# Kernel tuning notes

Hardware: AMD Instinct MI355X
Metric: run time of the kernel (lower is better)

The kernel has to match this reference:

```python
import jax, jax.numpy as jnp
import numpy as np

# --- fixed model configuration (from init_kwargs) ---
NX, NY, NU, NP = 8, 8, 2, 5
DELTA = 0.01
PHO, CP, AR, AB = 5.0, 6.0, 3.0, 3.0
KR, KB, TD, QR, QB = 2.5, 1.5, 300.0, 200.0, 200.0
CAF, TF = 6.0, 320.0
YMEAN = jnp.array([50.0, 1.0, 0.5, 313.0, 50.0, 1.0, 0.5, 313.0], jnp.float32)
YSTD = jnp.array([2.0, 0.2, 0.1, 4.0, 2.0, 0.2, 0.1, 4.0], jnp.float32)
UMEAN = jnp.array([10.0, 5.0], jnp.float32)
USTD = jnp.array([1.0, 0.5], jnp.float32)


def _fg(x, u):
    """Grey-box CSTR+flash ODE RHS. x: [B,8] scaled, u: [B,2] scaled."""
    x = x * YSTD + YMEAN
    u = u * USTD + UMEAN
    Hr, CAr, CBr, Tr = x[..., 0:1], x[..., 1:2], x[..., 2:3], x[..., 3:4]
    Hb, CAb, CBb, Tb = x[..., 4:5], x[..., 5:6], x[..., 6:7], x[..., 7:8]
    F, D = u[..., 0:1], u[..., 1:2]
    Fr = KR * jnp.sqrt(Hr)
    Fb = KB * jnp.sqrt(Hb)
    dHr = (F + D - Fr) / AR
    dCAr = (F * (CAF - CAr) - D * CAr) / (AR * Hr)
    dCBr = (-F * CBr - D * CBr) / (AR * Hr)
    dTr = (F * (TF - Tr) + D * (TD - Tr)) / (AR * Hr) + QR / (PHO * AR * CP * Hr)
    dHb = (Fr - Fb - D) / AB
    dCAb = (Fr * (CAr - CAb) + D * CAb) / (AB * Hb)
    dCBb = (Fr * (CBr - CBb) + D * CBb) / (AB * Hb)
    dTb = Fr * (Tr - Tb) / (AB * Hb) + QB / (PHO * AB * CP * Hb)
    xdot = jnp.concatenate([dHr, dCAr, dCBr, dTr, dHb, dCAb, dCBb, dTb], axis=-1)
    return xdot / YSTD


def setup_inputs() -> dict:
    key = jax.random.key(0)
    ks = jax.random.split(key, 6)
    B, T = 2048, 128
    d_in, d_h = NX + NP * (NY + NU) + NU, 128  # 60, 128
    useq = jax.random.normal(ks[0], (B, T, NU), jnp.float32)
    xGz0 = jax.random.normal(ks[1], (B, NX + NP * (NY + NU)), jnp.float32)
    W1 = jax.random.normal(ks[2], (d_in, d_h), jnp.float32) * (1.0 / np.sqrt(d_in))
    b1 = jnp.zeros((d_h,), jnp.float32)
    W2 = jax.random.normal(ks[3], (d_h, d_h), jnp.float32) * (1.0 / np.sqrt(d_h))
    b2 = jnp.zeros((d_h,), jnp.float32)
    W3 = jax.random.normal(ks[4], (d_h, NX), jnp.float32) * (1.0 / np.sqrt(d_h))
    b3 = jnp.zeros((NX,), jnp.float32)
    return {"useq": useq, "xGz0": xGz0, "W1": W1, "b1": b1,
            "W2": W2, "b2": b2, "W3": W3, "b3": b3}


def reference(useq, xGz0, W1, b1, W2, b2, W3, b3):
    def fnn(inp):
        h = jnp.tanh(inp @ W1 + b1)
        h = jnp.tanh(h @ W2 + b2)
        return h @ W3 + b3

    def interp(yfull):  # [B,(Np+1)*Ny] -> [B,Np*Ny]
        B = yfull.shape[0]
        y = yfull.reshape(B, NP + 1, NY)
        return (0.5 * (y[:, :-1] + y[:, 1:])).reshape(B, NP * NY)

    def step(xGz, u):
        xG = xGz[:, :NX]
        z = xGz[:, NX:]
        ypseq = z[:, :NP * NY]
        upseq = z[:, NP * NY:]
        # k1
        k1 = _fg(xG, u) + fnn(jnp.concatenate((xG, z, u), axis=-1))
        # interpolated half-step past sequence
        yp_interp = interp(jnp.concatenate((ypseq, xG), axis=-1))
        z_half = jnp.concatenate((yp_interp, upseq), axis=-1)
        x2 = xG + DELTA * (k1 / 2)
        k2 = _fg(x2, u) + fnn(jnp.concatenate((x2, z_half, u), axis=-1))
        x3 = xG + DELTA * (k2 / 2)
        k3 = _fg(x3, u) + fnn(jnp.concatenate((x3, z_half, u), axis=-1))
        yp_shift = jnp.concatenate((ypseq[:, NY:], xG), axis=-1)
        z_full = jnp.concatenate((yp_shift, upseq), axis=-1)
        x4 = xG + DELTA * k3
        k4 = _fg(x4, u) + fnn(jnp.concatenate((x4, z_full, u), axis=-1))
        y = xG
        xGplus = xG + (DELTA / 6) * (k1 + 2 * k2 + 2 * k3 + k4)
        zplus = jnp.concatenate((yp_shift, upseq[:, NU:], u), axis=-1)
        return jnp.concatenate((xGplus, zplus), axis=-1), y

    u_t = jnp.swapaxes(useq, 0, 1)  # [T,B,Nu]
    _, ys = jax.lax.scan(step, xGz0, u_t)  # ys: [T,B,Ny]
    return jnp.swapaxes(ys, 0, 1)  # [B,T,Ny]
```

## Files before the change

kernel.cpp:

```cpp
#include <hip/hip_runtime.h>
#include <math.h>

#define BLOCK 512
#define ROWS 8

typedef __attribute__((ext_vector_type(8))) short s16x8;
typedef __attribute__((ext_vector_type(4))) float f32x4;

static constexpr int O_H1   = 0;
static constexpr int O_H2   = 1088;
static constexpr int O_SU   = 2176;
static constexpr int O_PRIV = 4224;
static constexpr int PRIV_DW = 640;
static constexpr int LDSN  = O_PRIV + 8 * PRIV_DW;

__device__ __forceinline__ unsigned short f2bf(float f) {
  unsigned u = __float_as_uint(f);
  return (unsigned short)((u + 0x7fffu + ((u >> 16) & 1u)) >> 16);
}
__device__ __forceinline__ unsigned cvt_pk_bf16(float lo, float hi) {
  unsigned r;
  asm("v_cvt_pk_bf16_f32 %0, %1, %2" : "=v"(r) : "v"(lo), "v"(hi));
  return r;
}
__device__ __forceinline__ float tanh_fast(float x) {
  float e = __builtin_amdgcn_exp2f(x * 2.88539008177792681f);
  return fmaf(-2.f, __builtin_amdgcn_rcpf(e + 1.f), 1.f);
}

#define MFMA16(A, B, C) __builtin_amdgcn_mfma_f32_16x16x32_bf16((A), (B), (C), 0, 0, 0)

#define PACK_OUT(C, BV, DST) {                        \
  float t0_ = tanh_fast((C)[0] + (BV).x);             \
  float t1_ = tanh_fast((C)[1] + (BV).y);             \
  float t2_ = tanh_fast((C)[2] + (BV).z);             \
  float t3_ = tanh_fast((C)[3] + (BV).w);             \
  uint2 pk_; pk_.x = cvt_pk_bf16(t0_, t1_);           \
  pk_.y = cvt_pk_bf16(t2_, t3_);                      \
  *(uint2*)(DST) = pk_; }

extern "C" __global__ void __launch_bounds__(BLOCK, 1)
cstr_rk4_mfma6(const float* __restrict__ useq, const float* __restrict__ xGz0,
               const float* __restrict__ W1, const float* __restrict__ b1,
               const float* __restrict__ W2, const float* __restrict__ b2,
               const float* __restrict__ W3, const float* __restrict__ b3,
               float* __restrict__ out)
{
  extern __shared__ float smf[];
  unsigned short* h1h = (unsigned short*)(smf + O_H1);
  unsigned*       h1u = (unsigned*)(smf + O_H1);
  unsigned short* h2h = (unsigned short*)(smf + O_H2);
  unsigned*       h2u = (unsigned*)(smf + O_H2);
  float* su = smf + O_SU;

  const int tid  = threadIdx.x;
  const int w    = tid >> 6;
  const int l    = tid & 63;
  const int nn   = l & 15;
  const int hh   = l >> 4;
  const int r    = l >> 3;
  const int c    = l & 7;
  const int base = blockIdx.x * ROWS;

  float* wp_ = smf + O_PRIV + w * PRIV_DW;
  unsigned short* inhp = (unsigned short*)wp_;
  float* xmp = wp_ + 576;

  for (int i = tid; i < ROWS * 256; i += BLOCK) su[i] = useq[(size_t)base * 256 + i];
  for (int i = l; i < 16 * 72; i += 64) {
    int n_ = i / 72, k = i % 72;
    unsigned short v = 0;
    if (n_ < ROWS) {
      if (k < 58)      v = f2bf(xGz0[(size_t)(base + n_) * 58 + k]);
      else if (k < 60) v = f2bf(useq[(size_t)(base + n_) * 256 + (k - 58)]);
    }
    inhp[i] = v;
  }
  xmp[l] = xGz0[(size_t)(base + r) * 58 + c];

  const size_t rowb = (size_t)(base + r) * 58;
  float xg  = xGz0[rowb + c];
  float yp0 = xGz0[rowb + 8 + c],  yp1 = xGz0[rowb + 16 + c];
  float yp2 = xGz0[rowb + 24 + c], yp3 = xGz0[rowb + 32 + c];
  float yp4 = xGz0[rowb + 40 + c];
  float upA = xGz0[rowb + 48 + c];
  float upB = (c < 2) ? xGz0[rowb + 56 + c] : 0.f;
  float b3r = b3[c];
  float kacc = 0.f;

  const int j = 16 * w + nn;
  s16x8 a10, a11, a20, a21, a22, a23, a30, a31, a32, a33;
  #pragma unroll
  for (int i = 0; i < 8; ++i) {
    int k0 = 8 * hh + i, k1 = 32 + 8 * hh + i;
    a10[i] = (short)f2bf(W1[k0 * 128 + j]);
    a11[i] = (short)((k1 < 60) ? f2bf(W1[k1 * 128 + j]) : 0);
    a20[i] = (short)f2bf(W2[(     8 * hh + i) * 128 + j]);
    a21[i] = (short)f2bf(W2[(32 + 8 * hh + i) * 128 + j]);
    a22[i] = (short)f2bf(W2[(64 + 8 * hh + i) * 128 + j]);
    a23[i] = (short)f2bf(W2[(96 + 8 * hh + i) * 128 + j]);
    unsigned short z0 = 0, z1 = 0, z2 = 0, z3 = 0;
    if (nn < 8) {
      z0 = f2bf(W3[(     8 * hh + i) * 8 + nn]);
      z1 = f2bf(W3[(32 + 8 * hh + i) * 8 + nn]);
      z2 = f2bf(W3[(64 + 8 * hh + i) * 8 + nn]);
      z3 = f2bf(W3[(96 + 8 * hh + i) * 8 + nn]);
    }
    a30[i] = (short)z0; a31[i] = (short)z1; a32[i] = (short)z2; a33[i] = (short)z3;
  }
  const float4 bva = *(const float4*)(b1 + 16 * w + 4 * hh);
  const float4 bvb = *(const float4*)(b2 + 16 * w + 4 * hh);

  __syncthreads();

  const int srcl = ((c >> 2) << 4) + r;

  #pragma unroll 1
  for (int t = 0; t < 128; ++t) {
    const float u0r = su[r * 256 + 2 * t];
    const float u1r = su[r * 256 + 2 * t + 1];
    if (w == 0) out[((size_t)(base + r) * 128 + t) * 8 + c] = xg;

    #pragma unroll
    for (int s = 0; s < 4; ++s) {
      {
        s16x8 bb0 = *(const s16x8*)(inhp + nn * 72 + 8 * hh);
        s16x8 bb1 = *(const s16x8*)(inhp + nn * 72 + 32 + 8 * hh);
        f32x4 c1 = (f32x4){0.f, 0.f, 0.f, 0.f};
        c1 = MFMA16(a10, bb0, c1);
        c1 = MFMA16(a11, bb1, c1);
        PACK_OUT(c1, bva, h1u + nn * 68 + 8 * w + 2 * hh);
      }
      __syncthreads();

      {
        const unsigned short* h1row = h1h + nn * 136;
        s16x8 q0 = *(const s16x8*)(h1row +  0 + 8 * hh);
        s16x8 q1 = *(const s16x8*)(h1row + 32 + 8 * hh);
        s16x8 q2 = *(const s16x8*)(h1row + 64 + 8 * hh);
        s16x8 q3 = *(const s16x8*)(h1row + 96 + 8 * hh);
        f32x4 c2 = (f32x4){0.f, 0.f, 0.f, 0.f};
        c2 = MFMA16(a20, q0, c2); c2 = MFMA16(a21, q1, c2);
        c2 = MFMA16(a22, q2, c2); c2 = MFMA16(a23, q3, c2);
        PACK_OUT(c2, bvb, h2u + nn * 68 + 8 * w + 2 * hh);
      }
      __syncthreads();

      f32x4 c3 = (f32x4){0.f, 0.f, 0.f, 0.f};
      {
        const unsigned short* h2row = h2h + nn * 136;
        s16x8 p0 = *(const s16x8*)(h2row +  0 + 8 * hh);
        s16x8 p1 = *(const s16x8*)(h2row + 32 + 8 * hh);
        s16x8 p2 = *(const s16x8*)(h2row + 64 + 8 * hh);
        s16x8 p3 = *(const s16x8*)(h2row + 96 + 8 * hh);
        c3 = MFMA16(a30, p0, c3); c3 = MFMA16(a31, p1, c3);
        c3 = MFMA16(a32, p2, c3); c3 = MFMA16(a33, p3, c3);
      }
      float v0 = __shfl(c3[0], srcl);
      float v1 = __shfl(c3[1], srcl);
      float v2 = __shfl(c3[2], srcl);
      float v3 = __shfl(c3[3], srcl);
      {
        float nv = b3r + ((c & 2) ? ((c & 1) ? v3 : v2)
                                  : ((c & 1) ? v1 : v0));
        float4 xa = *(const float4*)(xmp + r * 8);
        float4 xb = *(const float4*)(xmp + r * 8 + 4);
        float Hr  = fmaf(xa.x, 2.f, 50.f),  CAr = fmaf(xa.y, 0.2f, 1.f);
        float CBr = fmaf(xa.z, 0.1f, 0.5f), Tr  = fmaf(xa.w, 4.f, 313.f);
        float Hb  = fmaf(xb.x, 2.f, 50.f),  CAb = fmaf(xb.y, 0.2f, 1.f);
        float CBb = fmaf(xb.z, 0.1f, 0.5f), Tb  = fmaf(xb.w, 4.f, 313.f);
        float F = u0r + 10.f, D = fmaf(u1r, 0.5f, 5.f);
        float Fr = 2.5f * sqrtf(Hr), Fb = 1.5f * sqrtf(Hb);
        float rH = __builtin_amdgcn_rcpf(3.f * Hr);
        float rB = __builtin_amdgcn_rcpf(3.f * Hb);
        float k0 = (F + D - Fr) * (1.f / 6.f);
        float k1 = (F * (6.f - CAr) - D * CAr) * (5.f * rH);
        float k2 = (-(F + D) * CBr) * (10.f * rH);
        float k3 = (F * (320.f - Tr) + D * (300.f - Tr)) * (0.25f * rH) + (5.f / 3.f) * rH;
        float k4 = (Fr - Fb - D) * (1.f / 6.f);
        float k5 = (Fr * (CAr - CAb) + D * CAb) * (5.f * rB);
        float k6 = (Fr * (CBr - CBb) + D * CBb) * (10.f * rB);
        float k7 = Fr * (Tr - Tb) * (0.25f * rB) + (5.f / 3.f) * rB;
        float fgc = (c & 4) ? ((c & 2) ? ((c & 1) ? k7 : k6) : ((c & 1) ? k5 : k4))
                            : ((c & 2) ? ((c & 1) ? k3 : k2) : ((c & 1) ? k1 : k0));
        float kv = fgc + nv;
        float cc;
        if (s == 0)      { kacc = kv;                  cc = fmaf(kv, 0.005f, xg); }
        else if (s == 1) { kacc = fmaf(kv, 2.f, kacc); cc = fmaf(kv, 0.005f, xg); }
        else if (s == 2) { kacc = fmaf(kv, 2.f, kacc); cc = fmaf(kv, 0.01f,  xg); }
        else             { xg = fmaf(kacc + kv, 0.01f / 6.f, xg); cc = xg; }
        xmp[r * 8 + c] = cc;
        inhp[r * 72 + c] = f2bf(cc);

        if (s == 0) {
          inhp[r * 72 +  8 + c] = f2bf(0.5f * (yp0 + yp1));
          inhp[r * 72 + 16 + c] = f2bf(0.5f * (yp1 + yp2));
          inhp[r * 72 + 24 + c] = f2bf(0.5f * (yp2 + yp3));
          inhp[r * 72 + 32 + c] = f2bf(0.5f * (yp3 + yp4));
          inhp[r * 72 + 40 + c] = f2bf(0.5f * (yp4 + xg));
        } else if (s == 2) {
          inhp[r * 72 +  8 + c] = f2bf(yp1);
          inhp[r * 72 + 16 + c] = f2bf(yp2);
          inhp[r * 72 + 24 + c] = f2bf(yp3);
          inhp[r * 72 + 32 + c] = f2bf(yp4);
          inhp[r * 72 + 40 + c] = f2bf(xg);
          yp0 = yp1; yp1 = yp2; yp2 = yp3; yp3 = yp4; yp4 = xg;
        } else if (s == 3) {
          float tA = __shfl(upA, r * 8 + ((c + 2) & 7));
          float tB = __shfl(upB, r * 8 + ((c >= 6) ? (c - 6) : 0));
          float nu = (c < 6) ? tA : tB;
          upA = nu;
          inhp[r * 72 + 48 + c] = f2bf(nu);
          if (c < 2) {
            float uv = (c == 0) ? u0r : u1r;
            upB = uv;
            inhp[r * 72 + 56 + c] = f2bf(uv);
            if (t < 127)
              inhp[r * 72 + 58 + c] = f2bf(su[r * 256 + 2 * (t + 1) + c]);
          }
        }
      }
    }
  }
}

extern "C" void kernel_launch(void* const* d_in, const int* in_sizes, int n_in,
                              void* d_out, int out_size, void* d_ws, size_t ws_size,
                              hipStream_t stream) {
  const float* useq = (const float*)d_in[0];
  const float* xGz0 = (const float*)d_in[1];
  const float* W1   = (const float*)d_in[2];
  const float* b1   = (const float*)d_in[3];
  const float* W2   = (const float*)d_in[4];
  const float* b2   = (const float*)d_in[5];
  const float* W3   = (const float*)d_in[6];
  const float* b3   = (const float*)d_in[7];
  float* out = (float*)d_out;

  size_t lds = (size_t)LDSN * sizeof(float);
  (void)hipFuncSetAttribute((const void*)cstr_rk4_mfma6,
                            hipFuncAttributeMaxDynamicSharedMemorySize, (int)lds);
  hipLaunchKernelGGL(cstr_rk4_mfma6, dim3(2048 / ROWS), dim3(BLOCK), lds, stream,
                     useq, xGz0, W1, b1, W2, b2, W3, b3, out);
}
```

Baseline: 541.6 us.

## Compute layer-3 and RK4 state update in one wave with shared input buffers

```diff
diff --git a/kernel.cpp b/kernel.cpp
--- a/kernel.cpp
+++ b/kernel.cpp
@@ -7,12 +7,12 @@
 typedef __attribute__((ext_vector_type(8))) short s16x8;
 typedef __attribute__((ext_vector_type(4))) float f32x4;
 
-static constexpr int O_H1   = 0;
-static constexpr int O_H2   = 1088;
-static constexpr int O_SU   = 2176;
-static constexpr int O_PRIV = 4224;
-static constexpr int PRIV_DW = 640;
-static constexpr int LDSN  = O_PRIV + 8 * PRIV_DW;
+static constexpr int O_H1  = 0;
+static constexpr int O_H2  = 1088;
+static constexpr int O_INH = 2176;
+static constexpr int O_XM  = 2752;
+static constexpr int O_SU  = 2816;
+static constexpr int LDSN  = 4896;
 
 __device__ __forceinline__ unsigned short f2bf(float f) {
   unsigned u = __float_as_uint(f);
@@ -40,7 +40,7 @@
   *(uint2*)(DST) = pk_; }
 
 extern "C" __global__ void __launch_bounds__(BLOCK, 1)
-cstr_rk4_mfma6(const float* __restrict__ useq, const float* __restrict__ xGz0,
+cstr_rk4_mfma7(const float* __restrict__ useq, const float* __restrict__ xGz0,
                const float* __restrict__ W1, const float* __restrict__ b1,
                const float* __restrict__ W2, const float* __restrict__ b2,
                const float* __restrict__ W3, const float* __restrict__ b3,
@@ -51,6 +51,8 @@
   unsigned*       h1u = (unsigned*)(smf + O_H1);
   unsigned short* h2h = (unsigned short*)(smf + O_H2);
   unsigned*       h2u = (unsigned*)(smf + O_H2);
+  unsigned short* inh = (unsigned short*)(smf + O_INH);
+  float* xm = smf + O_XM;
   float* su = smf + O_SU;
 
   const int tid  = threadIdx.x;
@@ -62,21 +64,20 @@
   const int c    = l & 7;
   const int base = blockIdx.x * ROWS;
 
-  float* wp_ = smf + O_PRIV + w * PRIV_DW;
-  unsigned short* inhp = (unsigned short*)wp_;
-  float* xmp = wp_ + 576;
-
-  for (int i = tid; i < ROWS * 256; i += BLOCK) su[i] = useq[(size_t)base * 256 + i];
-  for (int i = l; i < 16 * 72; i += 64) {
+  for (int i = tid; i < 8 * 260; i += BLOCK) {
+    int row = i / 260, col = i % 260;
+    su[i] = (col < 256) ? useq[(size_t)base * 256 + row * 256 + col] : 0.f;
+  }
+  for (int i = tid; i < 16 * 72; i += BLOCK) {
     int n_ = i / 72, k = i % 72;
     unsigned short v = 0;
     if (n_ < ROWS) {
       if (k < 58)      v = f2bf(xGz0[(size_t)(base + n_) * 58 + k]);
       else if (k < 60) v = f2bf(useq[(size_t)(base + n_) * 256 + (k - 58)]);
     }
-    inhp[i] = v;
-  }
-  xmp[l] = xGz0[(size_t)(base + r) * 58 + c];
+    inh[i] = v;
+  }
+  if (tid < 64) xm[tid] = xGz0[(size_t)(base + (tid >> 3)) * 58 + (tid & 7)];
 
   const size_t rowb = (size_t)(base + r) * 58;
   float xg  = xGz0[rowb + c];
@@ -117,15 +118,18 @@
 
   #pragma unroll 1
   for (int t = 0; t < 128; ++t) {
-    const float u0r = su[r * 256 + 2 * t];
-    const float u1r = su[r * 256 + 2 * t + 1];
-    if (w == 0) out[((size_t)(base + r) * 128 + t) * 8 + c] = xg;
+    float u0r = 0.f, u1r = 0.f;
+    if (w == 0) {
+      u0r = su[r * 260 + 2 * t];
+      u1r = su[r * 260 + 2 * t + 1];
+      out[((size_t)(base + r) * 128 + t) * 8 + c] = xg;
+    }
 
     #pragma unroll
     for (int s = 0; s < 4; ++s) {
       {
-        s16x8 bb0 = *(const s16x8*)(inhp + nn * 72 + 8 * hh);
-        s16x8 bb1 = *(const s16x8*)(inhp + nn * 72 + 32 + 8 * hh);
+        s16x8 bb0 = *(const s16x8*)(inh + nn * 72 + 8 * hh);
+        s16x8 bb1 = *(const s16x8*)(inh + nn * 72 + 32 + 8 * hh);
         f32x4 c1 = (f32x4){0.f, 0.f, 0.f, 0.f};
         c1 = MFMA16(a10, bb0, c1);
         c1 = MFMA16(a11, bb1, c1);
@@ -146,25 +150,26 @@
       }
       __syncthreads();
 
-      f32x4 c3 = (f32x4){0.f, 0.f, 0.f, 0.f};
-      {
-        const unsigned short* h2row = h2h + nn * 136;
-        s16x8 p0 = *(const s16x8*)(h2row +  0 + 8 * hh);
-        s16x8 p1 = *(const s16x8*)(h2row + 32 + 8 * hh);
-        s16x8 p2 = *(const s16x8*)(h2row + 64 + 8 * hh);
-        s16x8 p3 = *(const s16x8*)(h2row + 96 + 8 * hh);
-        c3 = MFMA16(a30, p0, c3); c3 = MFMA16(a31, p1, c3);
-        c3 = MFMA16(a32, p2, c3); c3 = MFMA16(a33, p3, c3);
-      }
-      float v0 = __shfl(c3[0], srcl);
-      float v1 = __shfl(c3[1], srcl);
-      float v2 = __shfl(c3[2], srcl);
-      float v3 = __shfl(c3[3], srcl);
-      {
+      if (w == 0) {
+        f32x4 c3 = (f32x4){0.f, 0.f, 0.f, 0.f};
+        {
+          const unsigned short* h2row = h2h + nn * 136;
+          s16x8 p0 = *(const s16x8*)(h2row +  0 + 8 * hh);
+          s16x8 p1 = *(const s16x8*)(h2row + 32 + 8 * hh);
+          s16x8 p2 = *(const s16x8*)(h2row + 64 + 8 * hh);
+          s16x8 p3 = *(const s16x8*)(h2row + 96 + 8 * hh);
+          c3 = MFMA16(a30, p0, c3); c3 = MFMA16(a31, p1, c3);
+          c3 = MFMA16(a32, p2, c3); c3 = MFMA16(a33, p3, c3);
+        }
+        float v0 = __shfl(c3[0], srcl);
+        float v1 = __shfl(c3[1], srcl);
+        float v2 = __shfl(c3[2], srcl);
+        float v3 = __shfl(c3[3], srcl);
+
         float nv = b3r + ((c & 2) ? ((c & 1) ? v3 : v2)
                                   : ((c & 1) ? v1 : v0));
-        float4 xa = *(const float4*)(xmp + r * 8);
-        float4 xb = *(const float4*)(xmp + r * 8 + 4);
+        float4 xa = *(const float4*)(xm + r * 8);
+        float4 xb = *(const float4*)(xm + r * 8 + 4);
         float Hr  = fmaf(xa.x, 2.f, 50.f),  CAr = fmaf(xa.y, 0.2f, 1.f);
         float CBr = fmaf(xa.z, 0.1f, 0.5f), Tr  = fmaf(xa.w, 4.f, 313.f);
         float Hb  = fmaf(xb.x, 2.f, 50.f),  CAb = fmaf(xb.y, 0.2f, 1.f);
@@ -189,37 +194,38 @@
         else if (s == 1) { kacc = fmaf(kv, 2.f, kacc); cc = fmaf(kv, 0.005f, xg); }
         else if (s == 2) { kacc = fmaf(kv, 2.f, kacc); cc = fmaf(kv, 0.01f,  xg); }
         else             { xg = fmaf(kacc + kv, 0.01f / 6.f, xg); cc = xg; }
-        xmp[r * 8 + c] = cc;
-        inhp[r * 72 + c] = f2bf(cc);
+        xm[r * 8 + c] = cc;
+        inh[r * 72 + c] = f2bf(cc);
 
         if (s == 0) {
-          inhp[r * 72 +  8 + c] = f2bf(0.5f * (yp0 + yp1));
-          inhp[r * 72 + 16 + c] = f2bf(0.5f * (yp1 + yp2));
-          inhp[r * 72 + 24 + c] = f2bf(0.5f * (yp2 + yp3));
-          inhp[r * 72 + 32 + c] = f2bf(0.5f * (yp3 + yp4));
-          inhp[r * 72 + 40 + c] = f2bf(0.5f * (yp4 + xg));
+          inh[r * 72 +  8 + c] = f2bf(0.5f * (yp0 + yp1));
+          inh[r * 72 + 16 + c] = f2bf(0.5f * (yp1 + yp2));
+          inh[r * 72 + 24 + c] = f2bf(0.5f * (yp2 + yp3));
+          inh[r * 72 + 32 + c] = f2bf(0.5f * (yp3 + yp4));
+          inh[r * 72 + 40 + c] = f2bf(0.5f * (yp4 + xg));
         } else if (s == 2) {
-          inhp[r * 72 +  8 + c] = f2bf(yp1);
-          inhp[r * 72 + 16 + c] = f2bf(yp2);
-          inhp[r * 72 + 24 + c] = f2bf(yp3);
-          inhp[r * 72 + 32 + c] = f2bf(yp4);
-          inhp[r * 72 + 40 + c] = f2bf(xg);
+          inh[r * 72 +  8 + c] = f2bf(yp1);
+          inh[r * 72 + 16 + c] = f2bf(yp2);
+          inh[r * 72 + 24 + c] = f2bf(yp3);
+          inh[r * 72 + 32 + c] = f2bf(yp4);
+          inh[r * 72 + 40 + c] = f2bf(xg);
           yp0 = yp1; yp1 = yp2; yp2 = yp3; yp3 = yp4; yp4 = xg;
         } else if (s == 3) {
           float tA = __shfl(upA, r * 8 + ((c + 2) & 7));
           float tB = __shfl(upB, r * 8 + ((c >= 6) ? (c - 6) : 0));
           float nu = (c < 6) ? tA : tB;
           upA = nu;
-          inhp[r * 72 + 48 + c] = f2bf(nu);
+          inh[r * 72 + 48 + c] = f2bf(nu);
           if (c < 2) {
             float uv = (c == 0) ? u0r : u1r;
             upB = uv;
-            inhp[r * 72 + 56 + c] = f2bf(uv);
+            inh[r * 72 + 56 + c] = f2bf(uv);
             if (t < 127)
-              inhp[r * 72 + 58 + c] = f2bf(su[r * 256 + 2 * (t + 1) + c]);
+              inh[r * 72 + 58 + c] = f2bf(su[r * 260 + 2 * (t + 1) + c]);
           }
         }
       }
+      __syncthreads();
     }
   }
 }
@@ -238,8 +244,8 @@
   float* out = (float*)d_out;
 
   size_t lds = (size_t)LDSN * sizeof(float);
-  (void)hipFuncSetAttribute((const void*)cstr_rk4_mfma6,
+  (void)hipFuncSetAttribute((const void*)cstr_rk4_mfma7,
                             hipFuncAttributeMaxDynamicSharedMemorySize, (int)lds);
-  hipLaunchKernelGGL(cstr_rk4_mfma6, dim3(2048 / ROWS), dim3(BLOCK), lds, stream,
+  hipLaunchKernelGGL(cstr_rk4_mfma7, dim3(2048 / ROWS), dim3(BLOCK), lds, stream,
                      useq, xGz0, W1, b1, W2, b2, W3, b3, out);
 }
```

Result: faster. 478.0 us (-11.7%).

## Fuse third-layer matmul into layer-2 epilogue via per-wave partial sums

Applied to the files above, without the earlier changes.

```diff
diff --git a/kernel.cpp b/kernel.cpp
--- a/kernel.cpp
+++ b/kernel.cpp
@@ -8,11 +8,11 @@
 typedef __attribute__((ext_vector_type(4))) float f32x4;
 
 static constexpr int O_H1   = 0;
-static constexpr int O_H2   = 1088;
-static constexpr int O_SU   = 2176;
-static constexpr int O_PRIV = 4224;
+static constexpr int O_SU   = 1088;
+static constexpr int O_PP   = 3168;
+static constexpr int O_PRIV = 3680;
 static constexpr int PRIV_DW = 640;
-static constexpr int LDSN  = O_PRIV + 8 * PRIV_DW;
+static constexpr int LDSN   = O_PRIV + 8 * PRIV_DW;
 
 __device__ __forceinline__ unsigned short f2bf(float f) {
   unsigned u = __float_as_uint(f);
@@ -30,17 +30,8 @@
 
 #define MFMA16(A, B, C) __builtin_amdgcn_mfma_f32_16x16x32_bf16((A), (B), (C), 0, 0, 0)
 
-#define PACK_OUT(C, BV, DST) {                        \
-  float t0_ = tanh_fast((C)[0] + (BV).x);             \
-  float t1_ = tanh_fast((C)[1] + (BV).y);             \
-  float t2_ = tanh_fast((C)[2] + (BV).z);             \
-  float t3_ = tanh_fast((C)[3] + (BV).w);             \
-  uint2 pk_; pk_.x = cvt_pk_bf16(t0_, t1_);           \
-  pk_.y = cvt_pk_bf16(t2_, t3_);                      \
-  *(uint2*)(DST) = pk_; }
-
 extern "C" __global__ void __launch_bounds__(BLOCK, 1)
-cstr_rk4_mfma6(const float* __restrict__ useq, const float* __restrict__ xGz0,
+cstr_rk4_mfma8(const float* __restrict__ useq, const float* __restrict__ xGz0,
                const float* __restrict__ W1, const float* __restrict__ b1,
                const float* __restrict__ W2, const float* __restrict__ b2,
                const float* __restrict__ W3, const float* __restrict__ b3,
@@ -49,9 +40,8 @@
   extern __shared__ float smf[];
   unsigned short* h1h = (unsigned short*)(smf + O_H1);
   unsigned*       h1u = (unsigned*)(smf + O_H1);
-  unsigned short* h2h = (unsigned short*)(smf + O_H2);
-  unsigned*       h2u = (unsigned*)(smf + O_H2);
   float* su = smf + O_SU;
+  float* pp = smf + O_PP;
 
   const int tid  = threadIdx.x;
   const int w    = tid >> 6;
@@ -66,7 +56,10 @@
   unsigned short* inhp = (unsigned short*)wp_;
   float* xmp = wp_ + 576;
 
-  for (int i = tid; i < ROWS * 256; i += BLOCK) su[i] = useq[(size_t)base * 256 + i];
+  for (int i = tid; i < 8 * 260; i += BLOCK) {
+    int row = i / 260, col = i % 260;
+    su[i] = (col < 256) ? useq[(size_t)base * 256 + row * 256 + col] : 0.f;
+  }
   for (int i = l; i < 16 * 72; i += 64) {
     int n_ = i / 72, k = i % 72;
     unsigned short v = 0;
@@ -89,7 +82,7 @@
   float kacc = 0.f;
 
   const int j = 16 * w + nn;
-  s16x8 a10, a11, a20, a21, a22, a23, a30, a31, a32, a33;
+  s16x8 a10, a11, a20, a21, a22, a23, a3h;
   #pragma unroll
   for (int i = 0; i < 8; ++i) {
     int k0 = 8 * hh + i, k1 = 32 + 8 * hh + i;
@@ -99,26 +92,19 @@
     a21[i] = (short)f2bf(W2[(32 + 8 * hh + i) * 128 + j]);
     a22[i] = (short)f2bf(W2[(64 + 8 * hh + i) * 128 + j]);
     a23[i] = (short)f2bf(W2[(96 + 8 * hh + i) * 128 + j]);
-    unsigned short z0 = 0, z1 = 0, z2 = 0, z3 = 0;
-    if (nn < 8) {
-      z0 = f2bf(W3[(     8 * hh + i) * 8 + nn]);
-      z1 = f2bf(W3[(32 + 8 * hh + i) * 8 + nn]);
-      z2 = f2bf(W3[(64 + 8 * hh + i) * 8 + nn]);
-      z3 = f2bf(W3[(96 + 8 * hh + i) * 8 + nn]);
-    }
-    a30[i] = (short)z0; a31[i] = (short)z1; a32[i] = (short)z2; a33[i] = (short)z3;
+    unsigned short z = 0;
+    if (i < 4 && nn < 8) z = f2bf(W3[(16 * w + 4 * hh + i) * 8 + nn]);
+    a3h[i] = (short)z;
   }
   const float4 bva = *(const float4*)(b1 + 16 * w + 4 * hh);
   const float4 bvb = *(const float4*)(b2 + 16 * w + 4 * hh);
 
   __syncthreads();
 
-  const int srcl = ((c >> 2) << 4) + r;
-
   #pragma unroll 1
   for (int t = 0; t < 128; ++t) {
-    const float u0r = su[r * 256 + 2 * t];
-    const float u1r = su[r * 256 + 2 * t + 1];
+    const float u0r = su[r * 260 + 2 * t];
+    const float u1r = su[r * 260 + 2 * t + 1];
     if (w == 0) out[((size_t)(base + r) * 128 + t) * 8 + c] = xg;
 
     #pragma unroll
@@ -129,7 +115,12 @@
         f32x4 c1 = (f32x4){0.f, 0.f, 0.f, 0.f};
         c1 = MFMA16(a10, bb0, c1);
         c1 = MFMA16(a11, bb1, c1);
-        PACK_OUT(c1, bva, h1u + nn * 68 + 8 * w + 2 * hh);
+        float t0 = tanh_fast(c1[0] + bva.x);
+        float t1 = tanh_fast(c1[1] + bva.y);
+        float t2 = tanh_fast(c1[2] + bva.z);
+        float t3 = tanh_fast(c1[3] + bva.w);
+        uint2 pk; pk.x = cvt_pk_bf16(t0, t1); pk.y = cvt_pk_bf16(t2, t3);
+        *(uint2*)(h1u + nn * 68 + 8 * w + 2 * hh) = pk;
       }
       __syncthreads();
 
@@ -142,27 +133,27 @@
         f32x4 c2 = (f32x4){0.f, 0.f, 0.f, 0.f};
         c2 = MFMA16(a20, q0, c2); c2 = MFMA16(a21, q1, c2);
         c2 = MFMA16(a22, q2, c2); c2 = MFMA16(a23, q3, c2);
-        PACK_OUT(c2, bvb, h2u + nn * 68 + 8 * w + 2 * hh);
+        float t0 = tanh_fast(c2[0] + bvb.x);
+        float t1 = tanh_fast(c2[1] + bvb.y);
+        float t2 = tanh_fast(c2[2] + bvb.z);
+        float t3 = tanh_fast(c2[3] + bvb.w);
+        s16x8 bf3;
+        ((unsigned*)&bf3)[0] = cvt_pk_bf16(t0, t1);
+        ((unsigned*)&bf3)[1] = cvt_pk_bf16(t2, t3);
+        ((unsigned*)&bf3)[2] = 0u;
+        ((unsigned*)&bf3)[3] = 0u;
+        f32x4 c3p = (f32x4){0.f, 0.f, 0.f, 0.f};
+        c3p = MFMA16(a3h, bf3, c3p);
+        if (nn < 8 && hh < 2)
+          *(float4*)(pp + w * 64 + nn * 8 + 4 * hh) =
+              make_float4(c3p[0], c3p[1], c3p[2], c3p[3]);
       }
       __syncthreads();
 
-      f32x4 c3 = (f32x4){0.f, 0.f, 0.f, 0.f};
       {
-        const unsigned short* h2row = h2h + nn * 136;
-        s16x8 p0 = *(const s16x8*)(h2row +  0 + 8 * hh);
-        s16x8 p1 = *(const s16x8*)(h2row + 32 + 8 * hh);
-        s16x8 p2 = *(const s16x8*)(h2row + 64 + 8 * hh);
-        s16x8 p3 = *(const s16x8*)(h2row + 96 + 8 * hh);
-        c3 = MFMA16(a30, p0, c3); c3 = MFMA16(a31, p1, c3);
-        c3 = MFMA16(a32, p2, c3); c3 = MFMA16(a33, p3, c3);
-      }
-      float v0 = __shfl(c3[0], srcl);
-      float v1 = __shfl(c3[1], srcl);
-      float v2 = __shfl(c3[2], srcl);
-      float v3 = __shfl(c3[3], srcl);
-      {
-        float nv = b3r + ((c & 2) ? ((c & 1) ? v3 : v2)
-                                  : ((c & 1) ? v1 : v0));
+        float nv = b3r;
+        #pragma unroll
+        for (int ww = 0; ww < 8; ++ww) nv += pp[ww * 64 + l];
         float4 xa = *(const float4*)(xmp + r * 8);
         float4 xb = *(const float4*)(xmp + r * 8 + 4);
         float Hr  = fmaf(xa.x, 2.f, 50.f),  CAr = fmaf(xa.y, 0.2f, 1.f);
@@ -216,7 +207,7 @@
             upB = uv;
             inhp[r * 72 + 56 + c] = f2bf(uv);
             if (t < 127)
-              inhp[r * 72 + 58 + c] = f2bf(su[r * 256 + 2 * (t + 1) + c]);
+              inhp[r * 72 + 58 + c] = f2bf(su[r * 260 + 2 * (t + 1) + c]);
           }
         }
       }
@@ -238,8 +229,8 @@
   float* out = (float*)d_out;
 
   size_t lds = (size_t)LDSN * sizeof(float);
-  (void)hipFuncSetAttribute((const void*)cstr_rk4_mfma6,
+  (void)hipFuncSetAttribute((const void*)cstr_rk4_mfma8,
                             hipFuncAttributeMaxDynamicSharedMemorySize, (int)lds);
-  hipLaunchKernelGGL(cstr_rk4_mfma6, dim3(2048 / ROWS), dim3(BLOCK), lds, stream,
+  hipLaunchKernelGGL(cstr_rk4_mfma8, dim3(2048 / ROWS), dim3(BLOCK), lds, stream,
                      useq, xGz0, W1, b1, W2, b2, W3, b3, out);
 }
```

Result: faster. 482.7 us (-10.9%).
